# Kernel optimization log

Hardware: AMD Instinct MI355X
Metric: run time of the kernel (lower is better)

## Reference

```python
import jax, jax.numpy as jnp
import numpy as np

D = 1024
H = 16
FF = 4 * D


def layer_norm(x, g, b, eps=1e-5):
    mu = jnp.mean(x, axis=-1, keepdims=True)
    var = jnp.var(x, axis=-1, keepdims=True)
    return (x - mu) * jax.lax.rsqrt(var + eps) * g + b


def setup_inputs() -> dict:
    key = jax.random.key(0)
    ks = jax.random.split(key, 8)
    s = lambda fan_in: 1.0 / np.sqrt(fan_in)
    return {
        "x": jax.random.normal(ks[0], (2, 2048, D), dtype=jnp.float32),
        "ln1_g": jnp.ones((D,), jnp.float32),
        "ln1_b": jnp.zeros((D,), jnp.float32),
        "w_qkv": jax.random.uniform(ks[1], (D, 3 * D), jnp.float32, -s(D), s(D)),
        "b_qkv": jnp.zeros((3 * D,), jnp.float32),
        "w_out": jax.random.uniform(ks[2], (D, D), jnp.float32, -s(D), s(D)),
        "b_out": jnp.zeros((D,), jnp.float32),
        "ln2_g": jnp.ones((D,), jnp.float32),
        "ln2_b": jnp.zeros((D,), jnp.float32),
        "w_fc1": jax.random.uniform(ks[3], (D, FF), jnp.float32, -s(D), s(D)),
        "b_fc1": jnp.zeros((FF,), jnp.float32),
        "w_fc2": jax.random.uniform(ks[4], (FF, D), jnp.float32, -s(FF), s(FF)),
        "b_fc2": jnp.zeros((D,), jnp.float32),
    }


def reference(x, ln1_g, ln1_b, w_qkv, b_qkv, w_out, b_out,
              ln2_g, ln2_b, w_fc1, b_fc1, w_fc2, b_fc2):
    b, n, c = x.shape
    hd = c // H
    scale = hd ** -0.5

    # --- pre-norm MHA ---
    h = layer_norm(x, ln1_g, ln1_b)
    qkv = h @ w_qkv + b_qkv                      # [b,n,3c]
    qkv = qkv.reshape(b, n, 3, H, hd)
    q = jnp.transpose(qkv[:, :, 0], (0, 2, 1, 3))  # [b,H,n,hd]
    k = jnp.transpose(qkv[:, :, 1], (0, 2, 1, 3))
    v = jnp.transpose(qkv[:, :, 2], (0, 2, 1, 3))
    attn = jnp.einsum('bhqd,bhkd->bhqk', q, k) * scale
    attn = jax.nn.softmax(attn, axis=-1)
    o = jnp.einsum('bhqk,bhkd->bhqd', attn, v)   # [b,H,n,hd]
    o = jnp.transpose(o, (0, 2, 1, 3)).reshape(b, n, c)
    x = x + (o @ w_out + b_out)

    # --- pre-norm FFN ---
    h = layer_norm(x, ln2_g, ln2_b)
    h = jax.nn.gelu(h @ w_fc1 + b_fc1, approximate=False)
    x = x + (h @ w_fc2 + b_fc2)
    return x
```

## Files before the change

### kernel.cpp

```cpp
#include <hip/hip_runtime.h>
#include <stdint.h>
#include <math.h>

#define D_MODEL 1024
#define NHEAD   16
#define HDIM    64
#define FFDIM   4096
#define SEQ     2048
#define BATCH   2
#define NTOK    (BATCH*SEQ)
#define QKVN    (3*D_MODEL)

typedef __bf16 bf16;
typedef __attribute__((ext_vector_type(8))) __bf16 bf16x8;
typedef __attribute__((ext_vector_type(4))) __bf16 bf16x4;
typedef __attribute__((ext_vector_type(4))) float f32x4;

__device__ __forceinline__ void gld_lds16(const void* g, void* l) {
    __builtin_amdgcn_global_load_lds((__attribute__((address_space(1))) void*)g,
                                     (__attribute__((address_space(3))) void*)l,
                                     16, 0, 0);
}

__device__ __forceinline__ float fast_exp2(float x) {
#if __has_builtin(__builtin_amdgcn_exp2f)
    return __builtin_amdgcn_exp2f(x);
#else
    return __expf(x * 0.69314718056f);
#endif
}

__global__ __launch_bounds__(256)
void k_transpose_all(const float* __restrict__ w_qkv, const float* __restrict__ w_out,
                     const float* __restrict__ w_fc1, const float* __restrict__ w_fc2,
                     bf16* __restrict__ t_qkv, bf16* __restrict__ t_out,
                     bf16* __restrict__ t_fc1, bf16* __restrict__ t_fc2) {
    __shared__ float tile[32][33];
    int bid = blockIdx.x;
    const float* W; bf16* Wt; int K, N, ti;
    if (bid < 3072)       { W = w_qkv; Wt = t_qkv; K = 1024; N = 3072; ti = bid; }
    else if (bid < 4096)  { W = w_out; Wt = t_out; K = 1024; N = 1024; ti = bid - 3072; }
    else if (bid < 8192)  { W = w_fc1; Wt = t_fc1; K = 1024; N = 4096; ti = bid - 4096; }
    else                  { W = w_fc2; Wt = t_fc2; K = 4096; N = 1024; ti = bid - 8192; }
    int tn = N >> 5;
    int n0 = (ti % tn) * 32, k0 = (ti / tn) * 32;
    int tx = threadIdx.x, ty = threadIdx.y;
#pragma unroll
    for (int i = 0; i < 4; i++)
        tile[ty + i * 8][tx] = W[(size_t)(k0 + ty + i * 8) * N + n0 + tx];
    __syncthreads();
#pragma unroll
    for (int i = 0; i < 4; i++)
        Wt[(size_t)(n0 + ty + i * 8) * K + k0 + tx] = (bf16)tile[tx][ty + i * 8];
}

__global__ __launch_bounds__(256)
void k_vtrans(const bf16* __restrict__ qkv, bf16* __restrict__ vT) {
    __shared__ bf16 t[32][33];
    int tok0 = blockIdx.x * 32, f0 = blockIdx.y * 32;
    int tx = threadIdx.x, ty = threadIdx.y;
#pragma unroll
    for (int i = 0; i < 4; i++)
        t[ty + i * 8][tx] = qkv[(size_t)(tok0 + ty + i * 8) * QKVN + 2 * D_MODEL + f0 + tx];
    __syncthreads();
    int s = tx;
    int pp = (s < 16) ? ((s >> 2) * 8 + (s & 3))
                      : (((s - 16) >> 2) * 8 + ((s - 16) & 3) + 4);
#pragma unroll
    for (int i = 0; i < 4; i++)
        vT[(size_t)(f0 + ty + i * 8) * NTOK + tok0 + pp] = t[tx][ty + i * 8];
}

__global__ __launch_bounds__(256)
void k_layernorm(const float* __restrict__ x, const float* __restrict__ g,
                 const float* __restrict__ b, bf16* __restrict__ out) {
    int row = blockIdx.x;
    int tid = threadIdx.x;
    float4 v = ((const float4*)(x + (size_t)row * D_MODEL))[tid];
    float s  = v.x + v.y + v.z + v.w;
    float ss = v.x * v.x + v.y * v.y + v.z * v.z + v.w * v.w;
#pragma unroll
    for (int off = 32; off > 0; off >>= 1) {
        s  += __shfl_down(s, off, 64);
        ss += __shfl_down(ss, off, 64);
    }
    __shared__ float red[2][4];
    __shared__ float mv[2];
    int wave = tid >> 6, lane = tid & 63;
    if (lane == 0) { red[0][wave] = s; red[1][wave] = ss; }
    __syncthreads();
    if (tid == 0) {
        float S  = red[0][0] + red[0][1] + red[0][2] + red[0][3];
        float SS = red[1][0] + red[1][1] + red[1][2] + red[1][3];
        float mu = S * (1.0f / D_MODEL);
        float var = SS * (1.0f / D_MODEL) - mu * mu;
        mv[0] = mu;
        mv[1] = rsqrtf(var + 1e-5f);
    }
    __syncthreads();
    float mu = mv[0], rs = mv[1];
    float4 gv = ((const float4*)g)[tid];
    float4 bv = ((const float4*)b)[tid];
    bf16x4 ov = { (bf16)((v.x - mu) * rs * gv.x + bv.x),
                  (bf16)((v.y - mu) * rs * gv.y + bv.y),
                  (bf16)((v.z - mu) * rs * gv.z + bv.z),
                  (bf16)((v.w - mu) * rs * gv.w + bv.w) };
    *(bf16x4*)(out + (size_t)row * D_MODEL + tid * 4) = ov;
}

template <int DO_GELU, int DO_RES, int OUT_BF16, int BN>
__global__ __launch_bounds__(256)
void k_gemm(const bf16* __restrict__ A, const bf16* __restrict__ Bt,
            const float* __restrict__ bias, const float* __restrict__ res,
            float* __restrict__ outf, bf16* __restrict__ outb,
            int M, int N, int K) {
    constexpr int WN = BN / 32;
    __shared__ bf16 As[128 * 32];
    __shared__ bf16 Bs[BN * 32];
    int tid  = threadIdx.x;
    int wave = tid >> 6, lane = tid & 63;
    int quad = lane >> 4, l16 = lane & 15;
    int m0 = blockIdx.y * 128, n0 = blockIdx.x * BN;
    int wm = (wave >> 1) * 64, wn = (wave & 1) * (BN / 2);

    f32x4 acc[4][WN];
#pragma unroll
    for (int i = 0; i < 4; i++)
#pragma unroll
        for (int j = 0; j < WN; j++) acc[i][j] = (f32x4){0.f, 0.f, 0.f, 0.f};

    int lrow = lane >> 2;
    int lcol = (lane & 3) * 8;
    const bf16* gA0 = A + (size_t)(m0 + wave * 32 + lrow) * K + lcol;
    const bf16* gA1 = gA0 + (size_t)16 * K;
    bf16* lA0 = As + wave * 1024;
    bf16* lA1 = lA0 + 512;

    const bf16* gB0;
    const bf16* gB1 = nullptr;
    bf16 *lB0, *lB1 = nullptr;
    if constexpr (BN == 128) {
        gB0 = Bt + (size_t)(n0 + wave * 32 + lrow) * K + lcol;
        gB1 = gB0 + (size_t)16 * K;
        lB0 = Bs + wave * 1024;
        lB1 = lB0 + 512;
    } else {
        gB0 = Bt + (size_t)(n0 + wave * 16 + lrow) * K + lcol;
        lB0 = Bs + wave * 512;
    }

    for (int k0 = 0; k0 < K; k0 += 32) {
        __syncthreads();
        gld_lds16(gA0 + k0, lA0);
        gld_lds16(gA1 + k0, lA1);
        gld_lds16(gB0 + k0, lB0);
        if constexpr (BN == 128) gld_lds16(gB1 + k0, lB1);
        __syncthreads();
        bf16x8 af[4], bfr[WN];
#pragma unroll
        for (int mi = 0; mi < 4; mi++)
            af[mi] = *(const bf16x8*)(As + (wm + mi * 16 + l16) * 32 + quad * 8);
#pragma unroll
        for (int ni = 0; ni < WN; ni++)
            bfr[ni] = *(const bf16x8*)(Bs + (wn + ni * 16 + l16) * 32 + quad * 8);
#pragma unroll
        for (int mi = 0; mi < 4; mi++)
#pragma unroll
            for (int ni = 0; ni < WN; ni++)
                acc[mi][ni] = __builtin_amdgcn_mfma_f32_16x16x32_bf16(af[mi], bfr[ni], acc[mi][ni], 0, 0, 0);
    }

#pragma unroll
    for (int mi = 0; mi < 4; mi++) {
        int row = m0 + wm + mi * 16 + quad * 4;
#pragma unroll
        for (int ni = 0; ni < WN; ni++) {
            int col = n0 + wn + ni * 16 + l16;
            float bb = bias[col];
#pragma unroll
            for (int r = 0; r < 4; r++) {
                float v = acc[mi][ni][r] + bb;
                if (DO_GELU) v = 0.5f * v * (1.0f + erff(v * 0.70710678118f));
                size_t idx = (size_t)(row + r) * N + col;
                if (DO_RES) v += res[idx];
                if (OUT_BF16) outb[idx] = (bf16)v;
                else          outf[idx] = v;
            }
        }
    }
}

__global__ __launch_bounds__(256)
void k_attention2(const bf16* __restrict__ qkv, const bf16* __restrict__ vT,
                  bf16* __restrict__ o) {
    __shared__ bf16 Ks[2][64][32];
    __shared__ bf16 Vs[2][64][32];

    int tid = threadIdx.x, wave = tid >> 6, lane = tid & 63;
    int quad = lane >> 4, l16 = lane & 15;
    int bh = blockIdx.y;
    int b = bh >> 4, h = bh & 15;
    int q0 = blockIdx.x * 64 + wave * 16;

    const bf16* Qb  = qkv + (size_t)b * SEQ * QKVN + h * HDIM;
    const bf16* Kb  = Qb + D_MODEL;
    const bf16* vTb = vT + (size_t)h * HDIM * NTOK + b * SEQ;

    const float QSCALE = 0.125f * 1.44269504089f;
    bf16x8 qf[2];
#pragma unroll
    for (int c = 0; c < 2; c++) {
        bf16x8 qraw = *(const bf16x8*)(Qb + (size_t)(q0 + l16) * QKVN + c * 32 + quad * 8);
#pragma unroll
        for (int i = 0; i < 8; i++) qf[c][i] = (bf16)((float)qraw[i] * QSCALE);
    }

    const bf16* gK0 = Kb + (size_t)(wave * 16 + (lane >> 2)) * QKVN + 0 * 32 + (lane & 3) * 8;
    const bf16* gK1 = gK0 + 32;
    const bf16* gV0 = vTb + (size_t)(wave * 16 + (lane >> 2)) * NTOK + (lane & 3) * 8;
    const bf16* gV1 = gV0 + 32;
    bf16* lK0 = &Ks[0][wave * 16][0];
    bf16* lK1 = &Ks[1][wave * 16][0];
    bf16* lV0 = &Vs[0][wave * 16][0];
    bf16* lV1 = &Vs[1][wave * 16][0];

    f32x4 oacc[4];
#pragma unroll
    for (int i = 0; i < 4; i++) oacc[i] = (f32x4){0.f, 0.f, 0.f, 0.f};
    float lsum = 0.f;

    for (int kv0 = 0; kv0 < SEQ; kv0 += 64) {
        __syncthreads();
        size_t koff = (size_t)kv0 * QKVN;
        gld_lds16(gK0 + koff, lK0);
        gld_lds16(gK1 + koff, lK1);
        gld_lds16(gV0 + kv0, lV0);
        gld_lds16(gV1 + kv0, lV1);
        __syncthreads();

        f32x4 s[4];
#pragma unroll
        for (int t = 0; t < 4; t++) {
            bf16x8 af0 = *(const bf16x8*)(&Ks[0][t * 16 + l16][quad * 8]);
            bf16x8 af1 = *(const bf16x8*)(&Ks[1][t * 16 + l16][quad * 8]);
            f32x4 z = (f32x4){0.f, 0.f, 0.f, 0.f};
            z = __builtin_amdgcn_mfma_f32_16x16x32_bf16(af0, qf[0], z, 0, 0, 0);
            z = __builtin_amdgcn_mfma_f32_16x16x32_bf16(af1, qf[1], z, 0, 0, 0);
            s[t] = z;
        }

        bf16x4 p[4];
#pragma unroll
        for (int t = 0; t < 4; t++)
#pragma unroll
            for (int r = 0; r < 4; r++) {
                float pf = fast_exp2(s[t][r]);
                lsum += pf;
                p[t][r] = (bf16)pf;
            }

#pragma unroll
        for (int tp = 0; tp < 2; tp++) {
            bf16x8 pa = __builtin_shufflevector(p[2 * tp], p[2 * tp + 1], 0, 1, 2, 3, 4, 5, 6, 7);
#pragma unroll
            for (int nt = 0; nt < 4; nt++) {
                bf16x8 vb = *(const bf16x8*)(&Vs[tp][nt * 16 + l16][quad * 8]);
                oacc[nt] = __builtin_amdgcn_mfma_f32_16x16x32_bf16(pa, vb, oacc[nt], 0, 0, 0);
            }
        }
    }

    lsum += __shfl_xor(lsum, 16, 64);
    lsum += __shfl_xor(lsum, 32, 64);
    float invl[4];
#pragma unroll
    for (int r = 0; r < 4; r++)
        invl[r] = 1.0f / __shfl(lsum, quad * 4 + r, 16);

#pragma unroll
    for (int nt = 0; nt < 4; nt++)
#pragma unroll
        for (int r = 0; r < 4; r++)
            o[(size_t)(b * SEQ + q0 + quad * 4 + r) * D_MODEL + h * HDIM + nt * 16 + l16] =
                (bf16)(oacc[nt][r] * invl[r]);
}

extern "C" void kernel_launch(void* const* d_in, const int* in_sizes, int n_in,
                              void* d_out, int out_size, void* d_ws, size_t ws_size,
                              hipStream_t stream) {
    const float* x     = (const float*)d_in[0];
    const float* ln1_g = (const float*)d_in[1];
    const float* ln1_b = (const float*)d_in[2];
    const float* w_qkv = (const float*)d_in[3];
    const float* b_qkv = (const float*)d_in[4];
    const float* w_out = (const float*)d_in[5];
    const float* b_out = (const float*)d_in[6];
    const float* ln2_g = (const float*)d_in[7];
    const float* ln2_b = (const float*)d_in[8];
    const float* w_fc1 = (const float*)d_in[9];
    const float* b_fc1 = (const float*)d_in[10];
    const float* w_fc2 = (const float*)d_in[11];
    const float* b_fc2 = (const float*)d_in[12];
    float* out = (float*)d_out;

    uintptr_t ws = (uintptr_t)d_ws;
    bf16* wt_qkv = (bf16*)(ws + 0);
    bf16* wt_out = (bf16*)(ws + 6291456);
    bf16* wt_fc1 = (bf16*)(ws + 8388608);
    bf16* wt_fc2 = (bf16*)(ws + 16777216);
    bf16* hbuf   = (bf16*)(ws + 25165824);
    bf16* vT     = hbuf;
    bf16* qkv    = (bf16*)(ws + 33554432);
    bf16* attn_o = (bf16*)(ws + 58720256);
    bf16* hgelu  = (bf16*)(ws + 33554432);

    k_transpose_all<<<12288, dim3(32, 8), 0, stream>>>(w_qkv, w_out, w_fc1, w_fc2,
                                                       wt_qkv, wt_out, wt_fc1, wt_fc2);

    k_layernorm<<<NTOK, 256, 0, stream>>>(x, ln1_g, ln1_b, hbuf);

    k_gemm<0, 0, 1, 128><<<dim3(QKVN / 128, NTOK / 128), 256, 0, stream>>>(
        hbuf, wt_qkv, b_qkv, nullptr, nullptr, qkv, NTOK, QKVN, D_MODEL);

    k_vtrans<<<dim3(NTOK / 32, D_MODEL / 32), dim3(32, 8), 0, stream>>>(qkv, vT);

    k_attention2<<<dim3(SEQ / 64, BATCH * NHEAD), 256, 0, stream>>>(qkv, vT, attn_o);

    k_gemm<0, 1, 0, 64><<<dim3(D_MODEL / 64, NTOK / 128), 256, 0, stream>>>(
        attn_o, wt_out, b_out, x, out, nullptr, NTOK, D_MODEL, D_MODEL);

    k_layernorm<<<NTOK, 256, 0, stream>>>(out, ln2_g, ln2_b, hbuf);

    k_gemm<1, 0, 1, 128><<<dim3(FFDIM / 128, NTOK / 128), 256, 0, stream>>>(
        hbuf, wt_fc1, b_fc1, nullptr, nullptr, hgelu, NTOK, FFDIM, D_MODEL);

    k_gemm<0, 1, 0, 64><<<dim3(D_MODEL / 64, NTOK / 128), 256, 0, stream>>>(
        hgelu, wt_fc2, b_fc2, out, out, nullptr, NTOK, D_MODEL, FFDIM);
}
```

Baseline: 394.5 us.

## Split-K the N=1024 GEMMs with BN=128 tiles and add partial-sum pass

The out-projection and FC2 GEMMs now use 128-wide N tiles with a 2-way split over K. The first K chunk writes the biased, residual-added result and the second writes raw partials to a scratch buffer. A new elementwise kernel then adds the partials into the output. This keeps the grid occupied with larger, more efficient tiles, at the cost of an extra fp32 write/read pass over a 16 MB buffer and two extra launches. The scratch buffers reuse workspace regions (qkv and transposed weights) that are already dead at that point.

```diff
diff --git a/kernel.cpp b/kernel.cpp
--- a/kernel.cpp
+++ b/kernel.cpp
@@ -108,11 +108,23 @@
     *(bf16x4*)(out + (size_t)row * D_MODEL + tid * 4) = ov;
 }
 
-template <int DO_GELU, int DO_RES, int OUT_BF16, int BN>
+__global__ __launch_bounds__(256)
+void k_addin(float* __restrict__ out, const float* __restrict__ p, int n4) {
+    int i = blockIdx.x * 256 + threadIdx.x;
+    if (i < n4) {
+        float4 o = ((const float4*)out)[i];
+        float4 q = ((const float4*)p)[i];
+        o.x += q.x; o.y += q.y; o.z += q.z; o.w += q.w;
+        ((float4*)out)[i] = o;
+    }
+}
+
+template <int DO_GELU, int DO_RES, int OUT_BF16, int BN, int SPLITK>
 __global__ __launch_bounds__(256)
 void k_gemm(const bf16* __restrict__ A, const bf16* __restrict__ Bt,
             const float* __restrict__ bias, const float* __restrict__ res,
             float* __restrict__ outf, bf16* __restrict__ outb,
+            float* __restrict__ pbuf,
             int M, int N, int K) {
     constexpr int WN = BN / 32;
     __shared__ bf16 As[128 * 32];
@@ -122,6 +134,8 @@
     int quad = lane >> 4, l16 = lane & 15;
     int m0 = blockIdx.y * 128, n0 = blockIdx.x * BN;
     int wm = (wave >> 1) * 64, wn = (wave & 1) * (BN / 2);
+    int kc = (SPLITK > 1) ? blockIdx.z : 0;
+    int kbeg = kc * (K / SPLITK), kend = kbeg + K / SPLITK;
 
     f32x4 acc[4][WN];
 #pragma unroll
@@ -149,7 +163,7 @@
         lB0 = Bs + wave * 512;
     }
 
-    for (int k0 = 0; k0 < K; k0 += 32) {
+    for (int k0 = kbeg; k0 < kend; k0 += 32) {
         __syncthreads();
         gld_lds16(gA0 + k0, lA0);
         gld_lds16(gA1 + k0, lA1);
@@ -179,12 +193,16 @@
             float bb = bias[col];
 #pragma unroll
             for (int r = 0; r < 4; r++) {
-                float v = acc[mi][ni][r] + bb;
-                if (DO_GELU) v = 0.5f * v * (1.0f + erff(v * 0.70710678118f));
                 size_t idx = (size_t)(row + r) * N + col;
-                if (DO_RES) v += res[idx];
-                if (OUT_BF16) outb[idx] = (bf16)v;
-                else          outf[idx] = v;
+                if (SPLITK > 1 && kc > 0) {
+                    pbuf[idx] = acc[mi][ni][r];
+                } else {
+                    float v = acc[mi][ni][r] + bb;
+                    if (DO_GELU) v = 0.5f * v * (1.0f + erff(v * 0.70710678118f));
+                    if (DO_RES) v += res[idx];
+                    if (OUT_BF16) outb[idx] = (bf16)v;
+                    else          outf[idx] = v;
+                }
             }
         }
     }
@@ -313,27 +331,31 @@
     bf16* qkv    = (bf16*)(ws + 33554432);
     bf16* attn_o = (bf16*)(ws + 58720256);
     bf16* hgelu  = (bf16*)(ws + 33554432);
+    float* pb_op  = (float*)(ws + 33554432);
+    float* pb_fc2 = (float*)(ws + 0);
 
     k_transpose_all<<<12288, dim3(32, 8), 0, stream>>>(w_qkv, w_out, w_fc1, w_fc2,
                                                        wt_qkv, wt_out, wt_fc1, wt_fc2);
 
     k_layernorm<<<NTOK, 256, 0, stream>>>(x, ln1_g, ln1_b, hbuf);
 
-    k_gemm<0, 0, 1, 128><<<dim3(QKVN / 128, NTOK / 128), 256, 0, stream>>>(
-        hbuf, wt_qkv, b_qkv, nullptr, nullptr, qkv, NTOK, QKVN, D_MODEL);
+    k_gemm<0, 0, 1, 128, 1><<<dim3(QKVN / 128, NTOK / 128), 256, 0, stream>>>(
+        hbuf, wt_qkv, b_qkv, nullptr, nullptr, qkv, nullptr, NTOK, QKVN, D_MODEL);
 
     k_vtrans<<<dim3(NTOK / 32, D_MODEL / 32), dim3(32, 8), 0, stream>>>(qkv, vT);
 
     k_attention2<<<dim3(SEQ / 64, BATCH * NHEAD), 256, 0, stream>>>(qkv, vT, attn_o);
 
-    k_gemm<0, 1, 0, 64><<<dim3(D_MODEL / 64, NTOK / 128), 256, 0, stream>>>(
-        attn_o, wt_out, b_out, x, out, nullptr, NTOK, D_MODEL, D_MODEL);
+    k_gemm<0, 1, 0, 128, 2><<<dim3(D_MODEL / 128, NTOK / 128, 2), 256, 0, stream>>>(
+        attn_o, wt_out, b_out, x, out, nullptr, pb_op, NTOK, D_MODEL, D_MODEL);
+    k_addin<<<(NTOK * D_MODEL / 4 + 255) / 256, 256, 0, stream>>>(out, pb_op, NTOK * D_MODEL / 4);
 
     k_layernorm<<<NTOK, 256, 0, stream>>>(out, ln2_g, ln2_b, hbuf);
 
-    k_gemm<1, 0, 1, 128><<<dim3(FFDIM / 128, NTOK / 128), 256, 0, stream>>>(
-        hbuf, wt_fc1, b_fc1, nullptr, nullptr, hgelu, NTOK, FFDIM, D_MODEL);
-
-    k_gemm<0, 1, 0, 64><<<dim3(D_MODEL / 64, NTOK / 128), 256, 0, stream>>>(
-        hgelu, wt_fc2, b_fc2, out, out, nullptr, NTOK, D_MODEL, FFDIM);
-}
+    k_gemm<1, 0, 1, 128, 1><<<dim3(FFDIM / 128, NTOK / 128), 256, 0, stream>>>(
+        hbuf, wt_fc1, b_fc1, nullptr, nullptr, hgelu, nullptr, NTOK, FFDIM, D_MODEL);
+
+    k_gemm<0, 1, 0, 128, 2><<<dim3(D_MODEL / 128, NTOK / 128, 2), 256, 0, stream>>>(
+        hgelu, wt_fc2, b_fc2, out, out, nullptr, pb_fc2, NTOK, D_MODEL, FFDIM);
+    k_addin<<<(NTOK * D_MODEL / 4 + 255) / 256, 256, 0, stream>>>(out, pb_fc2, NTOK * D_MODEL / 4);
+}
```

Result: slower. 416.0 us (+5.5%).

## Double-buffer GEMM LDS tiles with register-staged global prefetch

Applied to the files above, without the earlier changes.

Replaces the direct global-to-LDS loads, which needed two barriers per k-step, with a two-stage pipeline. The next k-tile is loaded into registers while the MFMAs run on the current LDS buffer, then stored into the alternate buffer, leaving one barrier per iteration. The aim is to hide global load latency behind compute. In exchange it doubles LDS use, raises register pressure, and gives up the direct-to-LDS load path.

```diff
diff --git a/kernel.cpp b/kernel.cpp
--- a/kernel.cpp
+++ b/kernel.cpp
@@ -115,8 +115,8 @@
             float* __restrict__ outf, bf16* __restrict__ outb,
             int M, int N, int K) {
     constexpr int WN = BN / 32;
-    __shared__ bf16 As[128 * 32];
-    __shared__ bf16 Bs[BN * 32];
+    __shared__ bf16 As[2][128 * 32];
+    __shared__ bf16 Bs[2][BN * 32];
     int tid  = threadIdx.x;
     int wave = tid >> 6, lane = tid & 63;
     int quad = lane >> 4, l16 = lane & 15;
@@ -133,36 +133,78 @@
     int lcol = (lane & 3) * 8;
     const bf16* gA0 = A + (size_t)(m0 + wave * 32 + lrow) * K + lcol;
     const bf16* gA1 = gA0 + (size_t)16 * K;
-    bf16* lA0 = As + wave * 1024;
-    bf16* lA1 = lA0 + 512;
-
     const bf16* gB0;
     const bf16* gB1 = nullptr;
-    bf16 *lB0, *lB1 = nullptr;
     if constexpr (BN == 128) {
         gB0 = Bt + (size_t)(n0 + wave * 32 + lrow) * K + lcol;
         gB1 = gB0 + (size_t)16 * K;
-        lB0 = Bs + wave * 1024;
-        lB1 = lB0 + 512;
     } else {
         gB0 = Bt + (size_t)(n0 + wave * 16 + lrow) * K + lcol;
-        lB0 = Bs + wave * 512;
-    }
-
-    for (int k0 = 0; k0 < K; k0 += 32) {
+    }
+
+    int wA0 = wave * 1024 + lane * 8;
+    int wA1 = wA0 + 512;
+    int wB0 = (BN == 128) ? (wave * 1024 + lane * 8) : (wave * 512 + lane * 8);
+    int wB1 = wB0 + 512;
+
+    {
+        bf16x8 rA0 = *(const bf16x8*)(gA0);
+        bf16x8 rA1 = *(const bf16x8*)(gA1);
+        bf16x8 rB0 = *(const bf16x8*)(gB0);
+        bf16x8 rB1;
+        if constexpr (BN == 128) rB1 = *(const bf16x8*)(gB1);
+        *(bf16x8*)(&As[0][wA0]) = rA0;
+        *(bf16x8*)(&As[0][wA1]) = rA1;
+        *(bf16x8*)(&Bs[0][wB0]) = rB0;
+        if constexpr (BN == 128) *(bf16x8*)(&Bs[0][wB1]) = rB1;
+    }
+    __syncthreads();
+
+    const bf16* curA = &As[0][0];
+    const bf16* curB = &Bs[0][0];
+    bf16* nxtA = &As[1][0];
+    bf16* nxtB = &Bs[1][0];
+
+    int niter = K / 32;
+    for (int t = 1; t < niter; t++) {
+        int k0 = t * 32;
+        bf16x8 rA0 = *(const bf16x8*)(gA0 + k0);
+        bf16x8 rA1 = *(const bf16x8*)(gA1 + k0);
+        bf16x8 rB0 = *(const bf16x8*)(gB0 + k0);
+        bf16x8 rB1;
+        if constexpr (BN == 128) rB1 = *(const bf16x8*)(gB1 + k0);
+
+        bf16x8 af[4], bfr[WN];
+#pragma unroll
+        for (int mi = 0; mi < 4; mi++)
+            af[mi] = *(const bf16x8*)(curA + (wm + mi * 16 + l16) * 32 + quad * 8);
+#pragma unroll
+        for (int ni = 0; ni < WN; ni++)
+            bfr[ni] = *(const bf16x8*)(curB + (wn + ni * 16 + l16) * 32 + quad * 8);
+#pragma unroll
+        for (int mi = 0; mi < 4; mi++)
+#pragma unroll
+            for (int ni = 0; ni < WN; ni++)
+                acc[mi][ni] = __builtin_amdgcn_mfma_f32_16x16x32_bf16(af[mi], bfr[ni], acc[mi][ni], 0, 0, 0);
+
+        *(bf16x8*)(nxtA + wA0) = rA0;
+        *(bf16x8*)(nxtA + wA1) = rA1;
+        *(bf16x8*)(nxtB + wB0) = rB0;
+        if constexpr (BN == 128) *(bf16x8*)(nxtB + wB1) = rB1;
         __syncthreads();
-        gld_lds16(gA0 + k0, lA0);
-        gld_lds16(gA1 + k0, lA1);
-        gld_lds16(gB0 + k0, lB0);
-        if constexpr (BN == 128) gld_lds16(gB1 + k0, lB1);
-        __syncthreads();
+
+        const bf16* tA = curA; curA = nxtA; nxtA = (bf16*)tA;
+        const bf16* tB = curB; curB = nxtB; nxtB = (bf16*)tB;
+    }
+
+    {
         bf16x8 af[4], bfr[WN];
 #pragma unroll
         for (int mi = 0; mi < 4; mi++)
-            af[mi] = *(const bf16x8*)(As + (wm + mi * 16 + l16) * 32 + quad * 8);
+            af[mi] = *(const bf16x8*)(curA + (wm + mi * 16 + l16) * 32 + quad * 8);
 #pragma unroll
         for (int ni = 0; ni < WN; ni++)
-            bfr[ni] = *(const bf16x8*)(Bs + (wn + ni * 16 + l16) * 32 + quad * 8);
+            bfr[ni] = *(const bf16x8*)(curB + (wn + ni * 16 + l16) * 32 + quad * 8);
 #pragma unroll
         for (int mi = 0; mi < 4; mi++)
 #pragma unroll
```

Result: faster. 364.6 us (-7.6%).
